# Kernel optimization log

Hardware: AMD Instinct MI355X
Metric: run time of the kernel (lower is better)

Reference implementation:

```python
import jax, jax.numpy as jnp
import numpy as np

N_NODES = 20000
N_EDGES = 160000
FEAT = 512
HEADS = 4
NEG_SLOPE = 0.2


def setup_inputs() -> dict:
    key = jax.random.key(0)
    ks = jax.random.split(key, 8)
    s = 1.0 / np.sqrt(FEAT)
    return {
        "x": jax.random.normal(ks[0], (N_NODES, FEAT), dtype=jnp.float32),
        "edge_index": jax.random.randint(ks[1], (2, N_EDGES), 0, N_NODES, dtype=jnp.int32),
        "W_l": jax.random.normal(ks[2], (FEAT, HEADS * FEAT), dtype=jnp.float32) * s,
        "W_r": jax.random.normal(ks[3], (FEAT, HEADS * FEAT), dtype=jnp.float32) * s,
        "att": jax.random.normal(ks[4], (HEADS, FEAT), dtype=jnp.float32) * s,
        "bias": jax.random.normal(ks[5], (FEAT,), dtype=jnp.float32) * 0.01,
        "W_cls": jax.random.normal(ks[6], (FEAT, 2), dtype=jnp.float32) * s,
        "b_cls": jnp.zeros((2,), dtype=jnp.float32),
    }


def reference(x, edge_index, W_l, W_r, att, bias, W_cls, b_cls):
    N = x.shape[0]
    H, C = att.shape
    # PyG GATv2Conv default: add self-loops
    loops = jnp.arange(N, dtype=edge_index.dtype)
    ei = jnp.concatenate([edge_index, jnp.stack([loops, loops])], axis=1)
    src, dst = ei[0], ei[1]  # message j -> i

    xl = (x @ W_l).reshape(N, H, C)  # source transform
    xr = (x @ W_r).reshape(N, H, C)  # target transform

    # GATv2 score: e_ij = att . LeakyReLU(xl_j + xr_i)   -> [E, H]
    u = xl[src] + xr[dst]                      # [E, H, C]
    e = jnp.einsum('ehc,hc->eh', jax.nn.leaky_relu(u, NEG_SLOPE), att)

    # segment softmax over incoming edges of each dst node
    m = jax.ops.segment_max(e, dst, num_segments=N)          # [N, H]
    alpha = jnp.exp(e - m[dst])
    denom = jax.ops.segment_sum(alpha, dst, num_segments=N)  # [N, H]
    alpha = alpha / denom[dst]

    # aggregate: out_i = sum_j alpha_ij * xl_j
    out = jax.ops.segment_sum(alpha[:, :, None] * xl[src], dst, num_segments=N)  # [N,H,C]
    out = out.mean(axis=1) + bias  # concat=False -> mean over heads, then bias

    return out @ W_cls + b_cls  # [N, num_classes]
```

## Files before the change

kernel.cpp:

```cpp
#include <hip/hip_runtime.h>
#include <hip/hip_bf16.h>

#define FEAT    512
#define HEADS   4
#define NEG     0.2f

typedef unsigned int uint;
typedef unsigned short ushort_t;
typedef __attribute__((ext_vector_type(8))) short bf16x8v;
typedef __attribute__((ext_vector_type(4))) float f32x4v;
typedef __attribute__((address_space(3))) uint lds_u32_t;
typedef __attribute__((address_space(1))) const uint g_u32_t;

__device__ inline float bf2f(ushort_t h) { return __uint_as_float(((uint)h) << 16); }
__device__ inline ushort_t f2bf(float f) {
    uint u = __float_as_uint(f);
    u += 0x7fff + ((u >> 16) & 1);
    return (ushort_t)(u >> 16);
}
__device__ inline float2 up2(uint d) {
    return make_float2(__uint_as_float(d << 16), __uint_as_float(d & 0xffff0000u));
}
__device__ inline float2 f2add(float2 a, float2 b) { return make_float2(a.x + b.x, a.y + b.y); }
__device__ inline float2 f2min0(float2 a) { return make_float2(fminf(a.x, 0.f), fminf(a.y, 0.f)); }
__device__ inline float2 f2fma(float2 a, float2 b, float2 c) {
    return make_float2(fmaf(a.x, b.x, c.x), fmaf(a.y, b.y, c.y));
}
__device__ inline float2 f2fmas(float s, float2 b, float2 c) {
    return make_float2(fmaf(s, b.x, c.x), fmaf(s, b.y, c.y));
}

__global__ void probe_dtype(const ushort_t* __restrict__ x, int* flag) {
    int lane = threadIdx.x;
    int hits = 0;
    for (int i = lane; i < 128; i += 64) {
        ushort_t w = x[2 * i];
        uint hb = (w >> 8) & 0x7f;
        hits += (hb >= 0x38 && hb <= 0x42) ? 1 : 0;
    }
    #pragma unroll
    for (int off = 32; off >= 1; off >>= 1) hits += __shfl_xor(hits, off);
    if (lane == 0) *flag = (hits >= 64) ? 1 : 0;
}

__global__ __launch_bounds__(256) void canon_kernel(const void* __restrict__ in,
                                                    ushort_t* __restrict__ outp,
                                                    const int* __restrict__ flag, long long n,
                                                    int skip_if_bf16) {
    int isbf = *flag;
    if (isbf && skip_if_bf16) return;
    long long i0 = ((long long)blockIdx.x * 256 + threadIdx.x) * 8;
    if (i0 + 8 <= n) {
        if (isbf) {
            *(uint4*)&outp[i0] = *(const uint4*)((const ushort_t*)in + i0);
        } else {
            const float* f = (const float*)in + i0;
            float4 a = *(const float4*)f, b = *(const float4*)(f + 4);
            ushort_t o[8] = {f2bf(a.x), f2bf(a.y), f2bf(a.z), f2bf(a.w),
                             f2bf(b.x), f2bf(b.y), f2bf(b.z), f2bf(b.w)};
            *(uint4*)&outp[i0] = *(uint4*)o;
        }
    } else {
        for (long long i = i0; i < n; ++i)
            outp[i] = isbf ? ((const ushort_t*)in)[i] : f2bf(((const float*)in)[i]);
    }
}

__global__ __launch_bounds__(256) void canon_small4(
    const void* a0, ushort_t* o0, int n0, const void* a1, ushort_t* o1, int n1,
    const void* a2, ushort_t* o2, int n2, const void* a3, ushort_t* o3, int n3,
    const int* __restrict__ flag) {
    int isbf = *flag;
    int idx = blockIdx.x * 256 + threadIdx.x;
    const void* srcs[4] = {a0, a1, a2, a3};
    ushort_t* dsts[4] = {o0, o1, o2, o3};
    int ns[4] = {n0, n1, n2, n3};
    #pragma unroll
    for (int k = 0; k < 4; ++k) {
        if (idx < ns[k]) {
            dsts[k][idx] = isbf ? ((const ushort_t*)srcs[k])[idx]
                                : f2bf(((const float*)srcs[k])[idx]);
            return;
        }
        idx -= ns[k];
    }
}

__global__ void hist_kernel(const int* __restrict__ dst, int* deg, int E, int N) {
    int i = blockIdx.x * blockDim.x + threadIdx.x;
    if (i < E) {
        int d = dst[i];
        if ((uint)d < (uint)N) atomicAdd(&deg[d], 1);
    }
}

__global__ __launch_bounds__(256) void scan1(const int* __restrict__ deg, int* __restrict__ part,
                                             int* __restrict__ bsum, int N) {
    __shared__ int tmp[256];
    int b = blockIdx.x, tid = threadIdx.x;
    int i0 = b * 1024 + tid * 4;
    int v[4] = {0, 0, 0, 0};
    if (i0 + 4 <= N) { int4 q = *(const int4*)&deg[i0]; v[0]=q.x+1; v[1]=q.y+1; v[2]=q.z+1; v[3]=q.w+1; }
    else { for (int j = 0; j < 4; ++j) v[j] = (i0 + j < N) ? deg[i0 + j] + 1 : 0; }
    int s0 = v[0], s1 = s0 + v[1], s2 = s1 + v[2], s3 = s2 + v[3];
    tmp[tid] = s3;
    __syncthreads();
    for (int off = 1; off < 256; off <<= 1) {
        int t = (tid >= off) ? tmp[tid - off] : 0;
        __syncthreads();
        tmp[tid] += t;
        __syncthreads();
    }
    int base = tid ? tmp[tid - 1] : 0;
    int e[4] = {base, base + s0, base + s1, base + s2};
    if (i0 + 4 <= N) { *(int4*)&part[i0] = make_int4(e[0], e[1], e[2], e[3]); }
    else { for (int j = 0; j < 4; ++j) if (i0 + j < N) part[i0 + j] = e[j]; }
    if (tid == 255) bsum[b] = tmp[255];
}

__global__ void scan2(int* __restrict__ bsum, int* __restrict__ offsN, int Nb) {
    int lane = threadIdx.x;
    int carry = 0;
    for (int base = 0; base < Nb; base += 64) {
        int idx = base + lane;
        int v = (idx < Nb) ? bsum[idx] : 0;
        int incl = v;
        #pragma unroll
        for (int off = 1; off < 64; off <<= 1) {
            int t = __shfl_up(incl, off);
            if (lane >= off) incl += t;
        }
        if (idx < Nb) bsum[idx] = carry + (incl - v);
        carry += __shfl(incl, 63);
    }
    if (lane == 0) *offsN = carry;
}

__global__ __launch_bounds__(256) void scan3(const int* __restrict__ part, const int* __restrict__ bsum,
                                             int* __restrict__ offsets, int* __restrict__ cursor, int N) {
    int b = blockIdx.x;
    int add = bsum[b];
    int i0 = b * 1024 + threadIdx.x * 4;
    #pragma unroll
    for (int j = 0; j < 4; ++j) {
        int i = i0 + j;
        if (i < N) { int o = part[i] + add; offsets[i] = o; cursor[i] = o; }
    }
}

__global__ void scatter_kernel(const int* __restrict__ src, const int* __restrict__ dst,
                               int* cursor, int* srcs, int E, int N) {
    int i = blockIdx.x * blockDim.x + threadIdx.x;
    if (i >= E + N) return;
    int s, d;
    if (i < E) { s = src[i]; d = dst[i]; }
    else       { s = i - E; d = i - E; }
    if ((uint)d >= (uint)N) return;
    int pos = atomicAdd(&cursor[d], 1);
    if ((uint)pos < (uint)(E + N)) srcs[pos] = s;
}

__global__ __launch_bounds__(256) void transpose_canon(const void* __restrict__ in,
                                                       ushort_t* __restrict__ outp,
                                                       const int* __restrict__ flag,
                                                       int K, int N) {
    __shared__ ushort_t t[64][72];
    int k0 = blockIdx.y * 64, n0 = blockIdx.x * 64;
    int tid = threadIdx.x;
    int r = tid >> 3;
    int c = (tid & 7) * 8;
    int isbf = *flag;
    #pragma unroll
    for (int p = 0; p < 2; ++p) {
        int row = r + p * 32;
        size_t base = (size_t)(k0 + row) * N + n0 + c;
        if (isbf) {
            *(uint4*)&t[row][c] = *(const uint4*)((const ushort_t*)in + base);
        } else {
            const float* f = (const float*)in + base;
            float4 a = *(const float4*)f, b = *(const float4*)(f + 4);
            ushort_t o[8] = {f2bf(a.x), f2bf(a.y), f2bf(a.z), f2bf(a.w),
                             f2bf(b.x), f2bf(b.y), f2bf(b.z), f2bf(b.w)};
            *(uint4*)&t[row][c] = *(uint4*)o;
        }
    }
    __syncthreads();
    #pragma unroll
    for (int p = 0; p < 2; ++p) {
        int row = r + p * 32;
        #pragma unroll
        for (int j = 0; j < 8; ++j)
            outp[(size_t)(n0 + row) * K + k0 + c + j] = t[c + j][row];
    }
}

__global__ __launch_bounds__(256) void gemm128(const ushort_t* A_bf, const ushort_t* A_cv,
                                               const int* __restrict__ flag,
                                               const ushort_t* __restrict__ Bt,
                                               ushort_t* __restrict__ C,
                                               int M, int Nn, int K) {
    __shared__ ushort_t As[2][128 * 32];
    __shared__ ushort_t Bs[2][128 * 32];
    const ushort_t* A = (*flag) ? A_bf : A_cv;
    int tid = threadIdx.x;
    int wave = tid >> 6, lane = tid & 63;
    int row0 = blockIdx.y * 128, col0 = blockIdx.x * 128;
    int wm = (wave >> 1) * 64, wn = (wave & 1) * 64;

    f32x4v acc[4][4];
    #pragma unroll
    for (int i = 0; i < 4; ++i)
        #pragma unroll
        for (int j = 0; j < 4; ++j) acc[i][j] = (f32x4v){0.f, 0.f, 0.f, 0.f};

    int fm = lane & 15, kq8 = (lane >> 4) * 8;

    const ushort_t* srcA[2]; ushort_t* dstA0[2]; ushort_t* dstA1[2];
    const ushort_t* srcB[2]; ushort_t* dstB0[2]; ushort_t* dstB1[2];
    #pragma unroll
    for (int i = 0; i < 2; ++i) {
        int p = (wave * 2 + i) * 64 + lane;
        int row = p >> 2, kp = p & 3;
        int gra = row0 + row; if (gra >= M) gra = M - 1;
        srcA[i] = &A[(size_t)gra * K + kp * 8];
        srcB[i] = &Bt[(size_t)(col0 + row) * K + kp * 8];
        dstA0[i] = &As[0][p * 8]; dstA1[i] = &As[1][p * 8];
        dstB0[i] = &Bs[0][p * 8]; dstB1[i] = &Bs[1][p * 8];
    }

    for (int k0 = 0; k0 < K; k0 += 64) {
        #pragma unroll
        for (int i = 0; i < 2; ++i) {
            __builtin_amdgcn_global_load_lds((g_u32_t*)srcA[i],        (lds_u32_t*)dstA0[i], 16, 0, 0);
            __builtin_amdgcn_global_load_lds((g_u32_t*)(srcA[i] + 32), (lds_u32_t*)dstA1[i], 16, 0, 0);
            __builtin_amdgcn_global_load_lds((g_u32_t*)srcB[i],        (lds_u32_t*)dstB0[i], 16, 0, 0);
            __builtin_amdgcn_global_load_lds((g_u32_t*)(srcB[i] + 32), (lds_u32_t*)dstB1[i], 16, 0, 0);
            srcA[i] += 64; srcB[i] += 64;
        }
        __syncthreads();

        #pragma unroll
        for (int panel = 0; panel < 2; ++panel) {
            bf16x8v af[4], bfr[4];
            #pragma unroll
            for (int mi = 0; mi < 4; ++mi)
                af[mi] = *(const bf16x8v*)&As[panel][(wm + mi * 16 + fm) * 32 + kq8];
            #pragma unroll
            for (int nj = 0; nj < 4; ++nj)
                bfr[nj] = *(const bf16x8v*)&Bs[panel][(wn + nj * 16 + fm) * 32 + kq8];
            #pragma unroll
            for (int mi = 0; mi < 4; ++mi)
                #pragma unroll
                for (int nj = 0; nj < 4; ++nj)
                    acc[mi][nj] = __builtin_amdgcn_mfma_f32_16x16x32_bf16(af[mi], bfr[nj], acc[mi][nj], 0, 0, 0);
        }
        __syncthreads();
    }

    int col = lane & 15, rq = (lane >> 4) * 4;
    #pragma unroll
    for (int mi = 0; mi < 4; ++mi) {
        #pragma unroll
        for (int r = 0; r < 4; ++r) {
            int gm = row0 + wm + mi * 16 + rq + r;
            if (gm < M) {
                #pragma unroll
                for (int nj = 0; nj < 4; ++nj)
                    C[(size_t)gm * Nn + col0 + wn + nj * 16 + col] = f2bf(acc[mi][nj][r]);
            }
        }
    }
}

__global__ __launch_bounds__(256) void gat_aggregate(
    const ushort_t* __restrict__ xl, int xl_stride,
    const ushort_t* __restrict__ xr, int xr_stride,
    const int* __restrict__ offsets, const int* __restrict__ srcs,
    const ushort_t* __restrict__ att, const ushort_t* __restrict__ bias,
    const ushort_t* __restrict__ Wc, const ushort_t* __restrict__ bc,
    float* __restrict__ out, int c0, int Cn, int N, int EN) {
    int bn = blockIdx.x;
    if (bn >= Cn) return;
    int n = c0 + bn;
    int tid = threadIdx.x;
    int h = tid >> 6, lane = tid & 63;
    int hoff = h * FEAT + lane * 8;

    __shared__ float sh[HEADS][FEAT];
    __shared__ float r0s[HEADS], r1s[HEADS];

    float2 xrr[4], attr[4];
    { uint4 q = *(const uint4*)&xr[(size_t)bn * xr_stride + hoff];
      xrr[0] = up2(q.x); xrr[1] = up2(q.y); xrr[2] = up2(q.z); xrr[3] = up2(q.w); }
    { uint4 q = *(const uint4*)&att[hoff];
      attr[0] = up2(q.x); attr[1] = up2(q.y); attr[2] = up2(q.z); attr[3] = up2(q.w); }

    int start = offsets[n], end = offsets[n + 1];
    start = max(0, min(start, EN));
    end   = max(start, min(end, EN));
    int deg = end - start;

    int sv = 0;
    if (lane < deg) sv = srcs[start + lane];

    float l = 0.f;
    float2 acc[4] = {{0.f,0.f},{0.f,0.f},{0.f,0.f},{0.f,0.f}};
    const ushort_t* xlh = xl + hoff;
    const float2 cneg = make_float2(NEG - 1.0f, NEG - 1.0f);

    auto getS = [&](int i) -> int {
        if (i < 0) i = 0;
        if (i >= deg) i = deg - 1;
        if (i < 0) i = 0;
        int s = (i < 64) ? __shfl(sv, i) : srcs[start + i];
        return ((uint)s >= (uint)N) ? 0 : s;
    };
    auto fetchPair = [&](int i0, uint4& q0, uint4& q1) {
        int s0 = getS(i0), s1 = getS(i0 + 1);
        q0 = *(const uint4*)(xlh + (size_t)s0 * xl_stride);
        q1 = *(const uint4*)(xlh + (size_t)s1 * xl_stride);
    };
    auto body = [&](uint4 q) {
        float2 v[4] = {up2(q.x), up2(q.y), up2(q.z), up2(q.w)};
        float2 p2 = make_float2(0.f, 0.f);
        #pragma unroll
        for (int j = 0; j < 4; ++j) {
            float2 u  = f2add(v[j], xrr[j]);
            float2 lr = f2fma(f2min0(u), cneg, u);
            p2 = f2fma(lr, attr[j], p2);
        }
        float p = p2.x + p2.y;
        #pragma unroll
        for (int off = 32; off >= 1; off >>= 1) p += __shfl_xor(p, off);
        float w = __expf(p);
        l += w;
        #pragma unroll
        for (int j = 0; j < 4; ++j) acc[j] = f2fmas(w, v[j], acc[j]);
    };

    uint4 a0, a1, b0, b1, q0, q1;
    fetchPair(0, a0, a1);
    fetchPair(2, b0, b1);
    for (int e = 0; e < deg; e += 2) {
        fetchPair(e + 4, q0, q1);
        body(a0);
        if (e + 1 < deg) body(a1);
        a0 = b0; a1 = b1; b0 = q0; b1 = q1;
    }

    float inv = 0.25f / fmaxf(l, 1e-35f);
    #pragma unroll
    for (int j = 0; j < 4; ++j) {
        sh[h][lane * 8 + 2 * j]     = acc[j].x * inv;
        sh[h][lane * 8 + 2 * j + 1] = acc[j].y * inv;
    }
    __syncthreads();

    float p0 = 0.f, p1 = 0.f;
    for (int c = tid; c < FEAT; c += 256) {
        float f = sh[0][c] + sh[1][c] + sh[2][c] + sh[3][c] + bf2f(bias[c]);
        uint w2 = *(const uint*)&Wc[c * 2];
        p0 = fmaf(f, bf2f((ushort_t)(w2 & 0xffff)), p0);
        p1 = fmaf(f, bf2f((ushort_t)(w2 >> 16)), p1);
    }
    #pragma unroll
    for (int off = 32; off >= 1; off >>= 1) {
        p0 += __shfl_xor(p0, off);
        p1 += __shfl_xor(p1, off);
    }
    if (lane == 0) { r0s[h] = p0; r1s[h] = p1; }
    __syncthreads();
    if (tid == 0) {
        out[(size_t)n * 2 + 0] = r0s[0] + r0s[1] + r0s[2] + r0s[3] + bf2f(bc[0]);
        out[(size_t)n * 2 + 1] = r1s[0] + r1s[1] + r1s[2] + r1s[3] + bf2f(bc[1]);
    }
}

extern "C" void kernel_launch(void* const* d_in, const int* in_sizes, int n_in,
                              void* d_out, int out_size, void* d_ws, size_t ws_size,
                              hipStream_t stream) {
    const void* x    = d_in[0];
    const int*  ei   = (const int*)d_in[1];
    const void* W_l  = d_in[2];
    const void* W_r  = d_in[3];
    const void* att  = d_in[4];
    const void* bias = d_in[5];
    const void* Wc   = d_in[6];
    const void* bc   = d_in[7];
    float* out = (float*)d_out;

    const int N  = in_sizes[0] / FEAT;
    const int E  = in_sizes[1] / 2;
    const int K  = FEAT;
    const int HC = HEADS * FEAT;
    const int EN = E + N;
    const int Nb = (N + 1023) / 1024;

    const int* src = ei;
    const int* dst = ei + E;

    char* base = (char*)d_ws;
    size_t off = 0;
    auto alloc = [&](size_t bytes) -> char* {
        char* p = base + off;
        off = (off + bytes + 255) & ~(size_t)255;
        return p;
    };
    int* flag    = (int*)alloc(4);
    int* offsets = (int*)alloc((size_t)(N + 1) * 4);
    int* cursor  = (int*)alloc((size_t)N * 4);
    int* deg     = (int*)alloc((size_t)N * 4);
    int* part    = (int*)alloc((size_t)N * 4);
    int* bsum    = (int*)alloc((size_t)(Nb + 1) * 4);
    int* srcs    = (int*)alloc((size_t)EN * 4);
    ushort_t* attc  = (ushort_t*)alloc((size_t)HC * 2);
    ushort_t* biasc = (ushort_t*)alloc((size_t)FEAT * 2);
    ushort_t* Wcc   = (ushort_t*)alloc((size_t)FEAT * 2 * 2);
    ushort_t* bcc   = (ushort_t*)alloc(2 * 2);
    ushort_t* xc   = (ushort_t*)alloc((size_t)N * K * 2);
    ushort_t* Wcat = (ushort_t*)alloc((size_t)2 * HC * K * 2);
    size_t fixed = off;

    size_t need_merged = (size_t)N * 2 * HC * 2;
    bool merged = (ws_size >= fixed + need_merged);

    probe_dtype<<<1, 64, 0, stream>>>((const ushort_t*)x, flag);
    long long NX = (long long)N * K;
    canon_kernel<<<(int)((NX + 2047) / 2048), 256, 0, stream>>>(x, xc, flag, NX, 1);
    canon_small4<<<15, 256, 0, stream>>>(att, attc, HC, bias, biasc, FEAT,
                                         Wc, Wcc, FEAT * 2, bc, bcc, 2, flag);

    hipMemsetAsync(deg, 0, (size_t)N * 4, stream);
    hist_kernel<<<(E + 255) / 256, 256, 0, stream>>>(dst, deg, E, N);
    scan1<<<Nb, 256, 0, stream>>>(deg, part, bsum, N);
    scan2<<<1, 64, 0, stream>>>(bsum, &offsets[N], Nb);
    scan3<<<Nb, 256, 0, stream>>>(part, bsum, offsets, cursor, N);
    scatter_kernel<<<(EN + 255) / 256, 256, 0, stream>>>(src, dst, cursor, srcs, E, N);

    dim3 tg(HC / 64, K / 64);
    transpose_canon<<<tg, 256, 0, stream>>>(W_l, Wcat, flag, K, HC);
    transpose_canon<<<tg, 256, 0, stream>>>(W_r, Wcat + (size_t)HC * K, flag, K, HC);

    const ushort_t* x_bf = (const ushort_t*)x;

    if (merged) {
        ushort_t* xlr = (ushort_t*)(base + fixed);
        dim3 gg(2 * HC / 128, (N + 127) / 128);
        gemm128<<<gg, 256, 0, stream>>>(x_bf, xc, flag, Wcat, xlr, N, 2 * HC, K);
        gat_aggregate<<<N, 256, 0, stream>>>(xlr, 2 * HC, xlr + HC, 2 * HC,
                                             offsets, srcs, attc, biasc, Wcc, bcc,
                                             out, 0, N, N, EN);
    } else {
        ushort_t* xl = (ushort_t*)alloc((size_t)N * HC * 2);
        size_t remain = (ws_size > off) ? (ws_size - off) : 0;
        long long Cmax = (long long)(remain / ((size_t)HC * 2));
        int C = (Cmax >= N) ? N : (int)(Cmax & ~63LL);
        if (C < 64) C = 64;
        ushort_t* xrc = (ushort_t*)(base + off);
        ushort_t* Wlt = Wcat;
        ushort_t* Wrt = Wcat + (size_t)HC * K;

        dim3 gl(HC / 128, (N + 127) / 128);
        gemm128<<<gl, 256, 0, stream>>>(x_bf, xc, flag, Wlt, xl, N, HC, K);
        for (int c0 = 0; c0 < N; c0 += C) {
            int Cn = (N - c0 < C) ? (N - c0) : C;
            dim3 gr(HC / 128, (Cn + 127) / 128);
            gemm128<<<gr, 256, 0, stream>>>(x_bf + (size_t)c0 * K, xc + (size_t)c0 * K, flag,
                                            Wrt, xrc, Cn, HC, K);
            gat_aggregate<<<Cn, 256, 0, stream>>>(xl, HC, xrc, HC,
                                                  offsets, srcs, attc, biasc, Wcc, bcc,
                                                  out, c0, Cn, N, EN);
        }
    }
}
```

Measured before the change: 351.0 us.

## Fuse scan stages and weight transposes, stage GEMM epilogue through LDS, precompute byte offsets

Folds the single-block scan2 into scan3, where each block rescans the up-to-64 block sums in one wave. The W_l and W_r transposes become one launch via blockIdx.z. The GEMM now writes its bf16 tile into a padded shared buffer and stores 16-byte rows, replacing scattered 2-byte global stores. The aggregation kernel precomputes 32-bit byte offsets for source rows so each gather needs less address arithmetic. The new scan assumes Nb <= 64, which holds for N=20000 but not in general.

```diff
diff --git a/kernel.cpp b/kernel.cpp
--- a/kernel.cpp
+++ b/kernel.cpp
@@ -118,34 +118,31 @@
     if (tid == 255) bsum[b] = tmp[255];
 }
 
-__global__ void scan2(int* __restrict__ bsum, int* __restrict__ offsN, int Nb) {
-    int lane = threadIdx.x;
-    int carry = 0;
-    for (int base = 0; base < Nb; base += 64) {
-        int idx = base + lane;
-        int v = (idx < Nb) ? bsum[idx] : 0;
+__global__ __launch_bounds__(256) void scan3(const int* __restrict__ part, const int* __restrict__ bsum,
+                                             int* __restrict__ offsets, int* __restrict__ cursor,
+                                             int N, int Nb) {
+    __shared__ int s_add, s_tot;
+    int b = blockIdx.x, tid = threadIdx.x;
+    if (tid < 64) {
+        int v = (tid < Nb) ? bsum[tid] : 0;
         int incl = v;
         #pragma unroll
         for (int off = 1; off < 64; off <<= 1) {
             int t = __shfl_up(incl, off);
-            if (lane >= off) incl += t;
-        }
-        if (idx < Nb) bsum[idx] = carry + (incl - v);
-        carry += __shfl(incl, 63);
-    }
-    if (lane == 0) *offsN = carry;
-}
-
-__global__ __launch_bounds__(256) void scan3(const int* __restrict__ part, const int* __restrict__ bsum,
-                                             int* __restrict__ offsets, int* __restrict__ cursor, int N) {
-    int b = blockIdx.x;
-    int add = bsum[b];
-    int i0 = b * 1024 + threadIdx.x * 4;
+            if (tid >= off) incl += t;
+        }
+        if (tid == b) s_add = incl - v;
+        if (tid == Nb - 1) s_tot = incl;
+    }
+    __syncthreads();
+    int add = s_add;
+    int i0 = b * 1024 + tid * 4;
     #pragma unroll
     for (int j = 0; j < 4; ++j) {
         int i = i0 + j;
         if (i < N) { int o = part[i] + add; offsets[i] = o; cursor[i] = o; }
     }
+    if (b == Nb - 1 && tid == 0) offsets[N] = s_tot;
 }
 
 __global__ void scatter_kernel(const int* __restrict__ src, const int* __restrict__ dst,
@@ -160,11 +157,15 @@
     if ((uint)pos < (uint)(E + N)) srcs[pos] = s;
 }
 
-__global__ __launch_bounds__(256) void transpose_canon(const void* __restrict__ in,
-                                                       ushort_t* __restrict__ outp,
-                                                       const int* __restrict__ flag,
-                                                       int K, int N) {
+__global__ __launch_bounds__(256) void transpose_canon2(const void* __restrict__ inL,
+                                                        const void* __restrict__ inR,
+                                                        ushort_t* __restrict__ outL,
+                                                        ushort_t* __restrict__ outR,
+                                                        const int* __restrict__ flag,
+                                                        int K, int N) {
     __shared__ ushort_t t[64][72];
+    const void* in = blockIdx.z ? inR : inL;
+    ushort_t* outp = blockIdx.z ? outR : outL;
     int k0 = blockIdx.y * 64, n0 = blockIdx.x * 64;
     int tid = threadIdx.x;
     int r = tid >> 3;
@@ -199,8 +200,10 @@
                                                const ushort_t* __restrict__ Bt,
                                                ushort_t* __restrict__ C,
                                                int M, int Nn, int K) {
-    __shared__ ushort_t As[2][128 * 32];
-    __shared__ ushort_t Bs[2][128 * 32];
+    constexpr int CSTR = 132;
+    __shared__ ushort_t SH[128 * CSTR];
+    ushort_t* As = SH;
+    ushort_t* Bs = SH + 8192;
     const ushort_t* A = (*flag) ? A_bf : A_cv;
     int tid = threadIdx.x;
     int wave = tid >> 6, lane = tid & 63;
@@ -224,8 +227,8 @@
         int gra = row0 + row; if (gra >= M) gra = M - 1;
         srcA[i] = &A[(size_t)gra * K + kp * 8];
         srcB[i] = &Bt[(size_t)(col0 + row) * K + kp * 8];
-        dstA0[i] = &As[0][p * 8]; dstA1[i] = &As[1][p * 8];
-        dstB0[i] = &Bs[0][p * 8]; dstB1[i] = &Bs[1][p * 8];
+        dstA0[i] = &As[p * 8]; dstA1[i] = &As[4096 + p * 8];
+        dstB0[i] = &Bs[p * 8]; dstB1[i] = &Bs[4096 + p * 8];
     }
 
     for (int k0 = 0; k0 < K; k0 += 64) {
@@ -244,10 +247,10 @@
             bf16x8v af[4], bfr[4];
             #pragma unroll
             for (int mi = 0; mi < 4; ++mi)
-                af[mi] = *(const bf16x8v*)&As[panel][(wm + mi * 16 + fm) * 32 + kq8];
+                af[mi] = *(const bf16x8v*)&As[panel * 4096 + (wm + mi * 16 + fm) * 32 + kq8];
             #pragma unroll
             for (int nj = 0; nj < 4; ++nj)
-                bfr[nj] = *(const bf16x8v*)&Bs[panel][(wn + nj * 16 + fm) * 32 + kq8];
+                bfr[nj] = *(const bf16x8v*)&Bs[panel * 4096 + (wn + nj * 16 + fm) * 32 + kq8];
             #pragma unroll
             for (int mi = 0; mi < 4; ++mi)
                 #pragma unroll
@@ -259,16 +262,20 @@
 
     int col = lane & 15, rq = (lane >> 4) * 4;
     #pragma unroll
-    for (int mi = 0; mi < 4; ++mi) {
-        #pragma unroll
-        for (int r = 0; r < 4; ++r) {
-            int gm = row0 + wm + mi * 16 + rq + r;
-            if (gm < M) {
-                #pragma unroll
-                for (int nj = 0; nj < 4; ++nj)
-                    C[(size_t)gm * Nn + col0 + wn + nj * 16 + col] = f2bf(acc[mi][nj][r]);
-            }
-        }
+    for (int mi = 0; mi < 4; ++mi)
+        #pragma unroll
+        for (int r = 0; r < 4; ++r)
+            #pragma unroll
+            for (int nj = 0; nj < 4; ++nj)
+                SH[(wm + mi * 16 + rq + r) * CSTR + wn + nj * 16 + col] = f2bf(acc[mi][nj][r]);
+    __syncthreads();
+    #pragma unroll
+    for (int j = 0; j < 8; ++j) {
+        int base = (tid + j * 256) * 8;
+        int r = base >> 7, c = base & 127;
+        int gm = row0 + r;
+        if (gm < M)
+            *(uint4*)&C[(size_t)gm * Nn + col0 + c] = *(const uint4*)&SH[r * CSTR + c];
     }
 }
 
@@ -300,25 +307,30 @@
     end   = max(start, min(end, EN));
     int deg = end - start;
 
-    int sv = 0;
-    if (lane < deg) sv = srcs[start + lane];
+    uint stride_b = (uint)xl_stride * 2u;
+    uint ov = 0;
+    if (lane < deg) {
+        int s = srcs[start + lane];
+        if ((uint)s < (uint)N) ov = (uint)s * stride_b;
+    }
 
     float l = 0.f;
     float2 acc[4] = {{0.f,0.f},{0.f,0.f},{0.f,0.f},{0.f,0.f}};
-    const ushort_t* xlh = xl + hoff;
+    const char* xlb = (const char*)(xl + hoff);
     const float2 cneg = make_float2(NEG - 1.0f, NEG - 1.0f);
 
-    auto getS = [&](int i) -> int {
-        if (i < 0) i = 0;
+    auto getO = [&](int i) -> uint {
         if (i >= deg) i = deg - 1;
         if (i < 0) i = 0;
-        int s = (i < 64) ? __shfl(sv, i) : srcs[start + i];
-        return ((uint)s >= (uint)N) ? 0 : s;
+        if (i < 64) return (uint)__shfl((int)ov, i);
+        int s = srcs[start + i];
+        if ((uint)s >= (uint)N) s = 0;
+        return (uint)s * stride_b;
     };
     auto fetchPair = [&](int i0, uint4& q0, uint4& q1) {
-        int s0 = getS(i0), s1 = getS(i0 + 1);
-        q0 = *(const uint4*)(xlh + (size_t)s0 * xl_stride);
-        q1 = *(const uint4*)(xlh + (size_t)s1 * xl_stride);
+        uint o0 = getO(i0), o1 = getO(i0 + 1);
+        q0 = *(const uint4*)(xlb + o0);
+        q1 = *(const uint4*)(xlb + o1);
     };
     auto body = [&](uint4 q) {
         float2 v[4] = {up2(q.x), up2(q.y), up2(q.z), up2(q.w)};
@@ -433,13 +445,12 @@
     hipMemsetAsync(deg, 0, (size_t)N * 4, stream);
     hist_kernel<<<(E + 255) / 256, 256, 0, stream>>>(dst, deg, E, N);
     scan1<<<Nb, 256, 0, stream>>>(deg, part, bsum, N);
-    scan2<<<1, 64, 0, stream>>>(bsum, &offsets[N], Nb);
-    scan3<<<Nb, 256, 0, stream>>>(part, bsum, offsets, cursor, N);
+    scan3<<<Nb, 256, 0, stream>>>(part, bsum, offsets, cursor, N, Nb);
     scatter_kernel<<<(EN + 255) / 256, 256, 0, stream>>>(src, dst, cursor, srcs, E, N);
 
-    dim3 tg(HC / 64, K / 64);
-    transpose_canon<<<tg, 256, 0, stream>>>(W_l, Wcat, flag, K, HC);
-    transpose_canon<<<tg, 256, 0, stream>>>(W_r, Wcat + (size_t)HC * K, flag, K, HC);
+    dim3 tg(HC / 64, K / 64, 2);
+    transpose_canon2<<<tg, 256, 0, stream>>>(W_l, W_r, Wcat, Wcat + (size_t)HC * K,
+                                             flag, K, HC);
 
     const ushort_t* x_bf = (const ushort_t*)x;
 
```

Result: no change. 353.4 us (+0.7%).
